# Optimization experiments

Measured on AMD Instinct MI355X. Metric: run time of the kernel, lower is better.

## Reference

```python
import jax, jax.numpy as jnp
import numpy as np
import math

D_MODEL = 1024
D_STATE = 128
D_CONV = 4
EXPAND = 2
HEADDIM = 64
NGROUPS = 1
CHUNK = 256
D_INNER = EXPAND * D_MODEL
D_SSM = D_INNER
NHEADS = D_SSM // HEADDIM
CONV_DIM = D_SSM + 2 * NGROUPS * D_STATE
D_IN_PROJ = 2 * D_INNER + 2 * NGROUPS * D_STATE + NHEADS
BATCH = 2
SEQLEN = 4096
EPS = 1e-5


def segsum(x):
    # x: (..., T) -> (..., T, T); segsum[i, j] = sum_{j < k <= i} x[k], -inf above diagonal
    T = x.shape[-1]
    xc = jnp.cumsum(x, axis=-1)
    d = xc[..., :, None] - xc[..., None, :]
    mask = jnp.tril(jnp.ones((T, T), dtype=bool))
    return jnp.where(mask, d, -jnp.inf)


def setup_inputs() -> dict:
    key = jax.random.key(0)
    ks = jax.random.split(key, 8)
    u = jax.random.normal(ks[0], (BATCH, SEQLEN, D_MODEL), jnp.float32)
    W_in = jax.random.normal(ks[1], (D_IN_PROJ, D_MODEL), jnp.float32) / np.sqrt(D_MODEL)
    conv_w = jax.random.uniform(ks[2], (CONV_DIM, D_CONV), jnp.float32, -1.0, 1.0) / np.sqrt(D_CONV)
    conv_b = jnp.zeros((CONV_DIM,), jnp.float32)
    # dt_bias init as in the torch module: inverse-softplus of dt ~ LogUniform(1e-3, 1e-1)
    dt = jnp.exp(jax.random.uniform(ks[3], (NHEADS,), jnp.float32) * (math.log(0.1) - math.log(0.001)) + math.log(0.001))
    dt = jnp.maximum(dt, 1e-4)
    dt_bias = dt + jnp.log(-jnp.expm1(-dt))
    A_log = jnp.log(jax.random.uniform(ks[4], (NHEADS,), jnp.float32, 1.0, 16.0))
    D = jnp.ones((NHEADS,), jnp.float32)
    norm_w = jnp.ones((D_SSM,), jnp.float32)
    W_out = jax.random.normal(ks[5], (D_MODEL, D_INNER), jnp.float32) / np.sqrt(D_INNER)
    return {"u": u, "W_in": W_in, "conv_w": conv_w, "conv_b": conv_b,
            "dt_bias": dt_bias, "A_log": A_log, "D": D, "norm_w": norm_w, "W_out": W_out}


def reference(u, W_in, conv_w, conv_b, dt_bias, A_log, D, norm_w, W_out):
    b, L, _ = u.shape
    zxbcdt = u @ W_in.T  # (b, L, d_in_proj); d_mlp == 0 for this config
    z, xBC, dt = jnp.split(zxbcdt, [D_SSM, D_SSM + CONV_DIM], axis=-1)

    # depthwise causal conv1d + SiLU (kernel width D_CONV, left padding)
    xpad = jnp.pad(xBC, ((0, 0), (D_CONV - 1, 0), (0, 0)))
    acc = conv_b
    for k in range(D_CONV):
        acc = acc + xpad[:, k:k + L, :] * conv_w[:, k]
    xBC = jax.nn.silu(acc)

    x, Bm, Cm = jnp.split(xBC, [D_SSM, D_SSM + NGROUPS * D_STATE], axis=-1)
    hpg = NHEADS // NGROUPS  # heads per B/C group
    Bh = jnp.repeat(Bm.reshape(b, L, NGROUPS, D_STATE), hpg, axis=2)  # (b, L, h, n)
    Ch = jnp.repeat(Cm.reshape(b, L, NGROUPS, D_STATE), hpg, axis=2)
    x = x.reshape(b, L, NHEADS, HEADDIM)

    dt = jax.nn.softplus(dt + dt_bias)  # (b, L, h)
    A = -jnp.exp(A_log)  # (h,)

    # ---- SSD chunked selective scan ----
    nc = L // CHUNK
    xc = x.reshape(b, nc, CHUNK, NHEADS, HEADDIM)
    Bc = Bh.reshape(b, nc, CHUNK, NHEADS, D_STATE)
    Cc = Ch.reshape(b, nc, CHUNK, NHEADS, D_STATE)
    dt_bclh = dt.reshape(b, nc, CHUNK, NHEADS)
    dA = jnp.transpose(dt_bclh, (0, 3, 1, 2)) * A[None, :, None, None]  # (b, h, c, l)
    A_cs = jnp.cumsum(dA, axis=-1)  # (b, h, c, l)

    # intra-chunk (diagonal block) outputs
    Ldiag = jnp.exp(segsum(dA))  # (b, h, c, l, s)
    x_dt = xc * dt_bclh[..., None]  # fold dt into x
    Y_diag = jnp.einsum('bclhn,bcshn,bhcls,bcshp->bclhp', Cc, Bc, Ldiag, x_dt)

    # per-chunk final states
    decay_states = jnp.exp(A_cs[..., -1:] - A_cs)  # (b, h, c, l)
    states = jnp.einsum('bclhn,bhcl,bclhp->bchpn', Bc, decay_states, x_dt)

    # inter-chunk recurrence via segsum over chunk-level decays
    chunk_sum = jnp.pad(A_cs[..., -1], ((0, 0), (0, 0), (1, 0)))  # (b, h, c+1)
    decay_chunk = jnp.exp(segsum(chunk_sum))  # (b, h, c+1, c+1)
    states = jnp.concatenate([jnp.zeros_like(states[:, :1]), states], axis=1)
    new_states = jnp.einsum('bhzc,bchpn->bzhpn', decay_chunk, states)
    prev_states = new_states[:, :-1]  # state entering each chunk

    # state -> output contribution
    Y_off = jnp.einsum('bclhn,bchpn,bhcl->bclhp', Cc, prev_states, jnp.exp(A_cs))

    y = (Y_diag + Y_off).reshape(b, L, NHEADS, HEADDIM) + x * D[None, None, :, None]
    y = y.reshape(b, L, D_SSM)

    # gated RMSNorm (norm_before_gate=False, ngroups=1 -> full-dim norm)
    y = y * jax.nn.silu(z)
    y = y * jax.lax.rsqrt(jnp.mean(jnp.square(y), axis=-1, keepdims=True) + EPS) * norm_w
    return y @ W_out.T
```

## Files before the change

### kernel.cpp

```cpp
#include <hip/hip_runtime.h>
#include <hip/hip_bf16.h>

#define ZX_LD   4384
#define XC_LD   2304
#define NH      32
#define HD      64
#define DS      128
#define CHK     256
#define NC      16
#define LTOT    4096
#define ROWS    8192
#define DSSM    2048
#define YPAD    80

typedef __bf16 bf16_t;
typedef bf16_t bf16x8 __attribute__((ext_vector_type(8)));
typedef float  f32x4  __attribute__((ext_vector_type(4)));
typedef unsigned short u16x8 __attribute__((ext_vector_type(8)));
typedef unsigned short u16x4 __attribute__((ext_vector_type(4)));

__device__ inline float bf2f(unsigned short u) {
  unsigned int x = ((unsigned int)u) << 16;
  float f; __builtin_memcpy(&f, &x, 4); return f;
}

#define GLOAD_LDS16(gp, lp) \
  __builtin_amdgcn_global_load_lds((const __attribute__((address_space(1))) void*)(gp), \
                                   (__attribute__((address_space(3))) void*)(lp), 16, 0, 0)

__global__ __launch_bounds__(256) void cast_f32_bf16(
    const float* __restrict__ in, bf16_t* __restrict__ out,
    long nvalid, long total)
{
  const long e0 = ((long)blockIdx.x * 256 + threadIdx.x) * 8;
  if (e0 >= total) return;
  bf16x8 o;
  if (e0 + 8 <= nvalid) {
    const float4 a = *(const float4*)(in + e0);
    const float4 b = *(const float4*)(in + e0 + 4);
    o[0]=(bf16_t)a.x; o[1]=(bf16_t)a.y; o[2]=(bf16_t)a.z; o[3]=(bf16_t)a.w;
    o[4]=(bf16_t)b.x; o[5]=(bf16_t)b.y; o[6]=(bf16_t)b.z; o[7]=(bf16_t)b.w;
  } else {
#pragma unroll
    for (int j = 0; j < 8; ++j) o[j] = (bf16_t)0.f;
  }
  *(bf16x8*)(out + e0) = o;
}

__global__ __launch_bounds__(256) void gemm_bt_mfma(
    const bf16_t* __restrict__ A, const bf16_t* __restrict__ B,
    float* __restrict__ C, int M, int N, int K,
    int lda, int ldb, int ldc)
{
  __shared__ __align__(16) bf16_t As[128 * 32];
  __shared__ __align__(16) bf16_t Bs[128 * 32];
  const int tid  = threadIdx.x;
  const int lane = tid & 63;
  const int wave = tid >> 6;

  const int nwg  = gridDim.x * gridDim.y;
  int wgid = blockIdx.y * gridDim.x + blockIdx.x;
  {
    const int xcd = wgid & 7, local = wgid >> 3;
    const int q = nwg >> 3, r = nwg & 7;
    wgid = (xcd < r ? xcd * (q + 1) : r * (q + 1) + (xcd - r) * q) + local;
  }
  const int bm = (wgid / gridDim.x) * 128;
  const int bn = (wgid % gridDim.x) * 128;

  const int wr = (wave >> 1) * 64;
  const int wc = (wave & 1) * 64;

  const int c0   = wave * 2;
  const int lrow = lane >> 2;
  const int lcol = (lane & 3) * 8;
  const bf16_t* Ag0 = A + (size_t)(bm + c0 * 16 + lrow) * lda + lcol;
  const bf16_t* Ag1 = A + (size_t)(bm + c0 * 16 + 16 + lrow) * lda + lcol;
  const bf16_t* Bg0 = B + (size_t)(bn + c0 * 16 + lrow) * ldb + lcol;
  const bf16_t* Bg1 = B + (size_t)(bn + c0 * 16 + 16 + lrow) * ldb + lcol;
  bf16_t* Al0 = As + c0 * 512;
  bf16_t* Al1 = As + c0 * 512 + 512;
  bf16_t* Bl0 = Bs + c0 * 512;
  bf16_t* Bl1 = Bs + c0 * 512 + 512;

  f32x4 acc[4][4];
#pragma unroll
  for (int i = 0; i < 4; ++i)
#pragma unroll
    for (int j = 0; j < 4; ++j) acc[i][j] = (f32x4){0.f, 0.f, 0.f, 0.f};

  const int nk = K >> 5;
  for (int kt = 0; kt < nk; ++kt) {
    const int k0 = kt * 32;
    __syncthreads();
    GLOAD_LDS16(Ag0 + k0, Al0);
    GLOAD_LDS16(Ag1 + k0, Al1);
    GLOAD_LDS16(Bg0 + k0, Bl0);
    GLOAD_LDS16(Bg1 + k0, Bl1);
    __syncthreads();

    const bf16_t* Ab = As + (wr + (lane & 15)) * 32 + (lane >> 4) * 8;
    const bf16_t* Bb = Bs + (wc + (lane & 15)) * 32 + (lane >> 4) * 8;
    bf16x8 af[4], bfv[4];
#pragma unroll
    for (int mi = 0; mi < 4; ++mi) af[mi]  = *(const bf16x8*)(Ab + mi * 512);
#pragma unroll
    for (int ni = 0; ni < 4; ++ni) bfv[ni] = *(const bf16x8*)(Bb + ni * 512);
#pragma unroll
    for (int mi = 0; mi < 4; ++mi)
#pragma unroll
      for (int ni = 0; ni < 4; ++ni)
        acc[mi][ni] = __builtin_amdgcn_mfma_f32_16x16x32_bf16(af[mi], bfv[ni], acc[mi][ni], 0, 0, 0);
  }

  const int crow0 = bm + wr + (lane >> 4) * 4;
  const int ccol0 = bn + wc + (lane & 15);
#pragma unroll
  for (int ni = 0; ni < 4; ++ni) {
    const int ccol = ccol0 + ni * 16;
    if (ccol < N) {
#pragma unroll
      for (int mi = 0; mi < 4; ++mi) {
#pragma unroll
        for (int j = 0; j < 4; ++j) {
          C[(size_t)(crow0 + mi * 16 + j) * ldc + ccol] = acc[mi][ni][j];
        }
      }
    }
  }
}

__global__ __launch_bounds__(256) void conv_silu_kernel(
    const float* __restrict__ zx, const float* __restrict__ cw,
    const float* __restrict__ cb, bf16_t* __restrict__ xconv)
{
  const int ch  = blockIdx.x * 256 + threadIdx.x;
  const int row = blockIdx.y;
  const int l   = row & (LTOT - 1);
  float acc = cb[ch];
#pragma unroll
  for (int k = 0; k < 4; ++k) {
    const int ls = l - 3 + k;
    if (ls >= 0) acc = fmaf(zx[(size_t)(row - 3 + k) * ZX_LD + 2048 + ch], cw[ch*4 + k], acc);
  }
  const float r = acc / (1.f + __expf(-acc));
  xconv[(size_t)row * XC_LD + ch] = (bf16_t)r;
}

__global__ __launch_bounds__(256) void dt_kernel(
    const float* __restrict__ zx, const float* __restrict__ dtb,
    float* __restrict__ dtv)
{
  const int idx = blockIdx.x * 256 + threadIdx.x;
  const int row = idx >> 5;
  const int hh  = idx & 31;
  const float x = zx[(size_t)row * ZX_LD + 4352 + hh] + dtb[hh];
  dtv[idx] = (x > 20.f) ? x : log1pf(__expf(x));
}

__global__ __launch_bounds__(256) void chunk_states_kernel(
    const float* __restrict__ dtv, const float* __restrict__ A_log,
    const bf16_t* __restrict__ xconv,
    float* __restrict__ acs, float* __restrict__ totals,
    float* __restrict__ states)
{
  const int bid = blockIdx.x;
  const int h = bid & 31;
  const int c = (bid >> 5) & 15;
  const int b = bid >> 9;
  const int rowbase = b * LTOT + c * CHK;
  const int tid = threadIdx.x;
  const int lane = tid & 63;
  const int wv   = tid >> 6;
  const int ln15 = lane & 15;
  const int lg   = lane >> 4;

  __shared__ float sWdt[256];
  __shared__ float wsum[4];
  __shared__ __align__(16) bf16_t xT[64 * 64];
  __shared__ __align__(16) bf16_t Bt[128 * 64];
  unsigned short* Btu = (unsigned short*)Bt;

  const float dt = dtv[(size_t)(rowbase + tid) * NH + h];
  const float Ah = -__expf(A_log[h]);
  float v = dt * Ah;
#pragma unroll
  for (int off = 1; off < 64; off <<= 1) {
    float up = __shfl_up(v, off, 64);
    if ((tid & 63) >= off) v += up;
  }
  if ((tid & 63) == 63) wsum[tid >> 6] = v;
  __syncthreads();
  const float w0 = wsum[0], w1 = wsum[1], w2 = wsum[2], w3 = wsum[3];
  float base = 0.f;
  if (wv > 0) base += w0;
  if (wv > 1) base += w1;
  if (wv > 2) base += w2;
  const float acsl  = v + base;
  const float total = w0 + w1 + w2 + w3;
  acs[bid * 256 + tid] = acsl;
  if (tid == 0) totals[(b * 32 + h) * 16 + c] = total;
  sWdt[tid] = __expf(total - acsl) * dt;

  f32x4 acc[4][2];
#pragma unroll
  for (int i = 0; i < 4; ++i)
#pragma unroll
    for (int j = 0; j < 2; ++j) acc[i][j] = (f32x4){0.f, 0.f, 0.f, 0.f};

  const int s  = tid >> 2;
  const int p0 = (tid & 3) * 16;
  const int n0 = (tid & 3) * 32;

  for (int ls = 0; ls < 4; ++ls) {
    const int l0 = ls * 64;
    __syncthreads();
    {
      const float wgt = sWdt[l0 + s];
      const bf16_t* xr = xconv + (size_t)(rowbase + l0 + s) * XC_LD + h * HD + p0;
      u16x8 v0 = *(const u16x8*)xr;
      u16x8 v1 = *(const u16x8*)(xr + 8);
#pragma unroll
      for (int j = 0; j < 8; ++j) {
        const int p = p0 + j;
        xT[p * 64 + ((((s >> 3) ^ (p & 7)) << 3) | (s & 7))] = (bf16_t)(bf2f(v0[j]) * wgt);
      }
#pragma unroll
      for (int j = 0; j < 8; ++j) {
        const int p = p0 + 8 + j;
        xT[p * 64 + ((((s >> 3) ^ (p & 7)) << 3) | (s & 7))] = (bf16_t)(bf2f(v1[j]) * wgt);
      }
      const bf16_t* br = xconv + (size_t)(rowbase + l0 + s) * XC_LD + 2048 + n0;
#pragma unroll
      for (int q = 0; q < 4; ++q) {
        u16x8 t = *(const u16x8*)(br + q * 8);
#pragma unroll
        for (int j = 0; j < 8; ++j) {
          const int n = n0 + q * 8 + j;
          Btu[n * 64 + ((((s >> 3) ^ (n & 7)) << 3) | (s & 7))] = t[j];
        }
      }
    }
    __syncthreads();
#pragma unroll
    for (int ks = 0; ks < 2; ++ks) {
      bf16x8 af[4];
#pragma unroll
      for (int mi = 0; mi < 4; ++mi) {
        const int row = mi * 16 + ln15;
        const int chunk = (ks * 4 + lg) ^ (row & 7);
        af[mi] = *(const bf16x8*)(xT + row * 64 + chunk * 8);
      }
#pragma unroll
      for (int ni = 0; ni < 2; ++ni) {
        const int nrow = wv * 32 + ni * 16 + ln15;
        const int chunk = (ks * 4 + lg) ^ (nrow & 7);
        bf16x8 bfr = *(const bf16x8*)(Bt + nrow * 64 + chunk * 8);
#pragma unroll
        for (int mi = 0; mi < 4; ++mi)
          acc[mi][ni] = __builtin_amdgcn_mfma_f32_16x16x32_bf16(af[mi], bfr, acc[mi][ni], 0, 0, 0);
      }
    }
  }

  const size_t sbase = (size_t)bid * (HD * DS);
#pragma unroll
  for (int mi = 0; mi < 4; ++mi) {
#pragma unroll
    for (int ni = 0; ni < 2; ++ni) {
      const int n = wv * 32 + ni * 16 + ln15;
#pragma unroll
      for (int j = 0; j < 4; ++j) {
        const int p = mi * 16 + lg * 4 + j;
        states[sbase + p * DS + n] = acc[mi][ni][j];
      }
    }
  }
}

__global__ __launch_bounds__(256) void chunk_prefix_kernel(
    const float* __restrict__ st, const float* __restrict__ totals,
    bf16_t* __restrict__ prevbf)
{
  const int bh = blockIdx.x;
  const int b = bh >> 5;
  const int h = bh & 31;
  const int e = blockIdx.y;
  const int tid = threadIdx.x;
  float P = 0.f;
  for (int c = 0; c < NC; ++c) {
    const size_t idx = (size_t)((b * 16 + c) * 32 + h) * (HD * DS) + e * 256 + tid;
    const float g = __expf(totals[bh * 16 + c]);
    prevbf[idx] = (bf16_t)P;
    P = fmaf(P, g, st[idx]);
  }
}

__global__ __launch_bounds__(256) void y_kernel_mfma(
    const bf16_t* __restrict__ xconv, const float* __restrict__ dtv,
    const float* __restrict__ acs,   const bf16_t* __restrict__ prevbf,
    const float* __restrict__ Dv,    float* __restrict__ ypre, int ypld)
{
  const int bid = blockIdx.x;
  const int lt = bid & 3;
  const int h  = (bid >> 2) & 31;
  const int c  = (bid >> 7) & 15;
  const int b  = bid >> 11;
  const int bch = (b * 16 + c) * 32 + h;
  const int rowbase = b * LTOT + c * CHK;
  const int tid  = threadIdx.x;
  const int lane = tid & 63;
  const int wv   = tid >> 6;
  const int ln15 = lane & 15;
  const int lg   = lane >> 4;

  __shared__ float sAcs[256];
  __shared__ float sDt[256];
  __shared__ __align__(16) bf16_t Cl[64 * 128];
  __shared__ __align__(16) bf16_t Bl[64 * 128];
  __shared__ __align__(16) bf16_t Sl[64 * YPAD];
  __shared__ __align__(16) bf16_t xT[64 * YPAD];
  unsigned short* xTu = (unsigned short*)xT;

  sAcs[tid] = acs[bch * 256 + tid];
  sDt[tid]  = dtv[(size_t)(rowbase + tid) * NH + h];

#pragma unroll
  for (int i = 0; i < 4; ++i) {
    const int chunk = wv * 4 + i;
    const int r  = chunk * 4 + lg;
    const int cs = ln15 ^ (r & 7);
    const bf16_t* src = xconv + (size_t)(rowbase + lt*64 + r) * XC_LD + 2176 + cs * 8;
    GLOAD_LDS16(src, Cl + chunk * 512);
  }
  __syncthreads();

  bf16x8 cf[4][4];
#pragma unroll
  for (int mi = 0; mi < 4; ++mi) {
    const int row = mi * 16 + ln15;
#pragma unroll
    for (int ks = 0; ks < 4; ++ks) {
      const int chunk = (ks * 4 + lg) ^ (row & 7);
      cf[mi][ks] = *(const bf16x8*)(Cl + row * 128 + chunk * 8);
    }
  }

  f32x4 acc[4];
#pragma unroll
  for (int mi = 0; mi < 4; ++mi) acc[mi] = (f32x4){0.f, 0.f, 0.f, 0.f};
  {
    const bf16_t* pb = prevbf + ((size_t)bch * 64 + 16 * wv + ln15) * 128 + lg * 8;
#pragma unroll
    for (int ks = 0; ks < 4; ++ks) {
      bf16x8 pf = *(const bf16x8*)(pb + ks * 32);
#pragma unroll
      for (int mi = 0; mi < 4; ++mi)
        acc[mi] = __builtin_amdgcn_mfma_f32_16x16x32_bf16(cf[mi][ks], pf, acc[mi], 0, 0, 0);
    }
  }
#pragma unroll
  for (int mi = 0; mi < 4; ++mi) {
#pragma unroll
    for (int j = 0; j < 4; ++j)
      acc[mi][j] *= __expf(sAcs[lt*64 + mi*16 + lg*4 + j]);
  }

  for (int st = 0; st <= lt; ++st) {
    __syncthreads();
#pragma unroll
    for (int i = 0; i < 4; ++i) {
      const int chunk = wv * 4 + i;
      const int r  = chunk * 4 + lg;
      const int cs = ln15 ^ (r & 7);
      const bf16_t* src = xconv + (size_t)(rowbase + st*64 + r) * XC_LD + 2048 + cs * 8;
      GLOAD_LDS16(src, Bl + chunk * 512);
    }
    {
      const int s  = tid >> 2;
      const int p0 = (tid & 3) * 16;
      const bf16_t* xr = xconv + (size_t)(rowbase + st*64 + s) * XC_LD + h * HD + p0;
      u16x8 v0 = *(const u16x8*)xr;
      u16x8 v1 = *(const u16x8*)(xr + 8);
#pragma unroll
      for (int j = 0; j < 8; ++j) xTu[(p0 + j) * YPAD + s] = v0[j];
#pragma unroll
      for (int j = 0; j < 8; ++j) xTu[(p0 + 8 + j) * YPAD + s] = v1[j];
    }
    __syncthreads();

    f32x4 sa[4];
#pragma unroll
    for (int mi = 0; mi < 4; ++mi) sa[mi] = (f32x4){0.f, 0.f, 0.f, 0.f};
    {
      const int row = 16 * wv + ln15;
#pragma unroll
      for (int ks = 0; ks < 4; ++ks) {
        const int chunk = (ks * 4 + lg) ^ (row & 7);
        bf16x8 bfr = *(const bf16x8*)(Bl + row * 128 + chunk * 8);
#pragma unroll
        for (int mi = 0; mi < 4; ++mi)
          sa[mi] = __builtin_amdgcn_mfma_f32_16x16x32_bf16(cf[mi][ks], bfr, sa[mi], 0, 0, 0);
      }
    }
    {
      const int sg = st * 64 + 16 * wv + ln15;
      const float as  = sAcs[sg];
      const float dts = sDt[sg];
#pragma unroll
      for (int mi = 0; mi < 4; ++mi) {
#pragma unroll
        for (int j = 0; j < 4; ++j) {
          const int lloc = mi * 16 + lg * 4 + j;
          const int ll = lt * 64 + lloc;
          float wvv = 0.f;
          if (ll >= sg) wvv = sa[mi][j] * __expf(sAcs[ll] - as) * dts;
          Sl[lloc * YPAD + 16 * wv + ln15] = (bf16_t)wvv;
        }
      }
    }
    __syncthreads();

#pragma unroll
    for (int ks2 = 0; ks2 < 2; ++ks2) {
      bf16x8 xf = *(const bf16x8*)(xT + (16 * wv + ln15) * YPAD + ks2 * 32 + lg * 8);
#pragma unroll
      for (int mi = 0; mi < 4; ++mi) {
        bf16x8 sf = *(const bf16x8*)(Sl + (mi * 16 + ln15) * YPAD + ks2 * 32 + lg * 8);
        acc[mi] = __builtin_amdgcn_mfma_f32_16x16x32_bf16(sf, xf, acc[mi], 0, 0, 0);
      }
    }
  }

  const float Dh = Dv[h];
  const int p = 16 * wv + ln15;
#pragma unroll
  for (int mi = 0; mi < 4; ++mi) {
#pragma unroll
    for (int j = 0; j < 4; ++j) {
      const int lloc = mi * 16 + lg * 4 + j;
      const int row  = rowbase + lt * 64 + lloc;
      const float xv = (float)xT[p * YPAD + lloc];
      ypre[(size_t)row * ypld + h * HD + p] = acc[mi][j] + xv * Dh;
    }
  }
}

__global__ __launch_bounds__(256) void rmsnorm_gate_kernel(
    const float* __restrict__ zx, const float* __restrict__ normw,
    bf16_t* __restrict__ ypre_bf)
{
  const int row = blockIdx.x;
  const int tid = threadIdx.x;
  float vals[8];
  float ss = 0.f;
#pragma unroll
  for (int e = 0; e < 8; ++e) {
    const int col = e * 256 + tid;
    const float y = zx[(size_t)row * ZX_LD + 2048 + col];
    const float z = zx[(size_t)row * ZX_LD + col];
    const float sz = z / (1.f + __expf(-z));
    const float v = y * sz;
    vals[e] = v;
    ss += v * v;
  }
#pragma unroll
  for (int off = 32; off >= 1; off >>= 1) ss += __shfl_xor(ss, off, 64);
  __shared__ float red[4];
  if ((tid & 63) == 0) red[tid >> 6] = ss;
  __syncthreads();
  const float tot = red[0] + red[1] + red[2] + red[3];
  const float scale = rsqrtf(tot / (float)DSSM + 1e-5f);
#pragma unroll
  for (int e = 0; e < 8; ++e) {
    const int col = e * 256 + tid;
    ypre_bf[(size_t)row * DSSM + col] = (bf16_t)(vals[e] * scale * normw[col]);
  }
}

extern "C" void kernel_launch(void* const* d_in, const int* in_sizes, int n_in,
                              void* d_out, int out_size, void* d_ws, size_t ws_size,
                              hipStream_t stream)
{
  const float* u       = (const float*)d_in[0];
  const float* W_in    = (const float*)d_in[1];
  const float* conv_w  = (const float*)d_in[2];
  const float* conv_b  = (const float*)d_in[3];
  const float* dt_bias = (const float*)d_in[4];
  const float* A_log   = (const float*)d_in[5];
  const float* Dv      = (const float*)d_in[6];
  const float* norm_w  = (const float*)d_in[7];
  const float* W_out   = (const float*)d_in[8];
  float* out = (float*)d_out;

  const size_t OFF_XC  = (size_t)ROWS * ZX_LD * 4;
  const size_t OFF_DT  = OFF_XC  + (size_t)ROWS * XC_LD * 2;
  const size_t OFF_ACS = OFF_DT  + (size_t)ROWS * NH * 4;
  const size_t OFF_TOT = OFF_ACS + (size_t)1024 * 256 * 4;
  const size_t OFF_ST  = OFF_TOT + 4096;
  const size_t OFF_AR  = OFF_ST  + (size_t)1024 * HD * DS * 4;
  const size_t need    = OFF_AR  + (size_t)ROWS * XC_LD * 2;
  if (ws_size < need) return;

  char* w = (char*)d_ws;
  float*  zx      = (float*)w;
  bf16_t* xconv   = (bf16_t*)(w + OFF_XC);
  float*  dtv     = (float*)(w + OFF_DT);
  float*  acsb    = (float*)(w + OFF_ACS);
  float*  totals  = (float*)(w + OFF_TOT);
  float*  states  = (float*)(w + OFF_ST);
  bf16_t* arena   = (bf16_t*)(w + OFF_AR);
  bf16_t* u_bf    = arena;
  bf16_t* Wpad    = arena + (size_t)ROWS * 1024;
  bf16_t* prevbf  = arena;
  bf16_t* ypre_bf = arena;
  bf16_t* Wout_bf = arena + (size_t)ROWS * DSSM;
  float*  ypre    = zx + 2048;

  {
    const long n_u = (long)ROWS * 1024;
    cast_f32_bf16<<<dim3((n_u/8 + 255)/256), 256, 0, stream>>>(u, u_bf, n_u, n_u);
    const long n_wv = (long)4384 * 1024, n_wt = (long)4480 * 1024;
    cast_f32_bf16<<<dim3((n_wt/8 + 255)/256), 256, 0, stream>>>(W_in, Wpad, n_wv, n_wt);
    const long n_wo = (long)1024 * DSSM;
    cast_f32_bf16<<<dim3((n_wo/8 + 255)/256), 256, 0, stream>>>(W_out, Wout_bf, n_wo, n_wo);
  }
  gemm_bt_mfma<<<dim3(35, 64), 256, 0, stream>>>(u_bf, Wpad, zx, ROWS, 4384, 1024,
                                                 1024, 1024, ZX_LD);
  conv_silu_kernel<<<dim3(9, ROWS), 256, 0, stream>>>(zx, conv_w, conv_b, xconv);
  dt_kernel<<<dim3((ROWS * NH) / 256), 256, 0, stream>>>(zx, dt_bias, dtv);
  chunk_states_kernel<<<dim3(1024), 256, 0, stream>>>(dtv, A_log, xconv, acsb, totals, states);
  chunk_prefix_kernel<<<dim3(64, 32), 256, 0, stream>>>(states, totals, prevbf);
  y_kernel_mfma<<<dim3(4096), 256, 0, stream>>>(xconv, dtv, acsb, prevbf, Dv, ypre, ZX_LD);
  rmsnorm_gate_kernel<<<dim3(ROWS), 256, 0, stream>>>(zx, norm_w, ypre_bf);
  gemm_bt_mfma<<<dim3(8, 64), 256, 0, stream>>>(ypre_bf, Wout_bf, out, ROWS, 1024, 2048,
                                                2048, 2048, 1024);
}
```

Baseline: 525.2 us.

## Store in_proj output and y intermediate in bf16, drop LDS staging in y kernel

The in_proj GEMM now writes its zxbcdt result as bf16 instead of fp32, halving the intermediate buffer. The conv, dt, y and rmsnorm kernels read and write bf16 versions of it. The rmsnorm kernel switches to vectorised 8-wide loads and stores. The y kernel drops its LDS staging for C and B and loads MFMA operands straight from global memory, removing one barrier per step. This cuts memory traffic but loses precision in z, dt and the y intermediate, and direct global fragment loads may be less coalesced than the previous staged path.

```diff
diff --git a/kernel.cpp b/kernel.cpp
--- a/kernel.cpp
+++ b/kernel.cpp
@@ -17,7 +17,6 @@
 typedef bf16_t bf16x8 __attribute__((ext_vector_type(8)));
 typedef float  f32x4  __attribute__((ext_vector_type(4)));
 typedef unsigned short u16x8 __attribute__((ext_vector_type(8)));
-typedef unsigned short u16x4 __attribute__((ext_vector_type(4)));
 
 __device__ inline float bf2f(unsigned short u) {
   unsigned int x = ((unsigned int)u) << 16;
@@ -47,9 +46,10 @@
   *(bf16x8*)(out + e0) = o;
 }
 
+template<bool BF16OUT>
 __global__ __launch_bounds__(256) void gemm_bt_mfma(
     const bf16_t* __restrict__ A, const bf16_t* __restrict__ B,
-    float* __restrict__ C, int M, int N, int K,
+    void* __restrict__ Cv, int M, int N, int K,
     int lda, int ldb, int ldc)
 {
   __shared__ __align__(16) bf16_t As[128 * 32];
@@ -123,7 +123,11 @@
       for (int mi = 0; mi < 4; ++mi) {
 #pragma unroll
         for (int j = 0; j < 4; ++j) {
-          C[(size_t)(crow0 + mi * 16 + j) * ldc + ccol] = acc[mi][ni][j];
+          if constexpr (BF16OUT) {
+            ((bf16_t*)Cv)[(size_t)(crow0 + mi * 16 + j) * ldc + ccol] = (bf16_t)acc[mi][ni][j];
+          } else {
+            ((float*)Cv)[(size_t)(crow0 + mi * 16 + j) * ldc + ccol] = acc[mi][ni][j];
+          }
         }
       }
     }
@@ -131,7 +135,7 @@
 }
 
 __global__ __launch_bounds__(256) void conv_silu_kernel(
-    const float* __restrict__ zx, const float* __restrict__ cw,
+    const bf16_t* __restrict__ zx, const float* __restrict__ cw,
     const float* __restrict__ cb, bf16_t* __restrict__ xconv)
 {
   const int ch  = blockIdx.x * 256 + threadIdx.x;
@@ -141,20 +145,21 @@
 #pragma unroll
   for (int k = 0; k < 4; ++k) {
     const int ls = l - 3 + k;
-    if (ls >= 0) acc = fmaf(zx[(size_t)(row - 3 + k) * ZX_LD + 2048 + ch], cw[ch*4 + k], acc);
+    if (ls >= 0)
+      acc = fmaf((float)zx[(size_t)(row - 3 + k) * ZX_LD + 2048 + ch], cw[ch*4 + k], acc);
   }
   const float r = acc / (1.f + __expf(-acc));
   xconv[(size_t)row * XC_LD + ch] = (bf16_t)r;
 }
 
 __global__ __launch_bounds__(256) void dt_kernel(
-    const float* __restrict__ zx, const float* __restrict__ dtb,
+    const bf16_t* __restrict__ zx, const float* __restrict__ dtb,
     float* __restrict__ dtv)
 {
   const int idx = blockIdx.x * 256 + threadIdx.x;
   const int row = idx >> 5;
   const int hh  = idx & 31;
-  const float x = zx[(size_t)row * ZX_LD + 4352 + hh] + dtb[hh];
+  const float x = (float)zx[(size_t)row * ZX_LD + 4352 + hh] + dtb[hh];
   dtv[idx] = (x > 20.f) ? x : log1pf(__expf(x));
 }
 
@@ -299,7 +304,7 @@
 __global__ __launch_bounds__(256) void y_kernel_mfma(
     const bf16_t* __restrict__ xconv, const float* __restrict__ dtv,
     const float* __restrict__ acs,   const bf16_t* __restrict__ prevbf,
-    const float* __restrict__ Dv,    float* __restrict__ ypre, int ypld)
+    const float* __restrict__ Dv,    bf16_t* __restrict__ ypre, int ypld)
 {
   const int bid = blockIdx.x;
   const int lt = bid & 3;
@@ -316,34 +321,20 @@
 
   __shared__ float sAcs[256];
   __shared__ float sDt[256];
-  __shared__ __align__(16) bf16_t Cl[64 * 128];
-  __shared__ __align__(16) bf16_t Bl[64 * 128];
   __shared__ __align__(16) bf16_t Sl[64 * YPAD];
   __shared__ __align__(16) bf16_t xT[64 * YPAD];
   unsigned short* xTu = (unsigned short*)xT;
 
   sAcs[tid] = acs[bch * 256 + tid];
   sDt[tid]  = dtv[(size_t)(rowbase + tid) * NH + h];
-
-#pragma unroll
-  for (int i = 0; i < 4; ++i) {
-    const int chunk = wv * 4 + i;
-    const int r  = chunk * 4 + lg;
-    const int cs = ln15 ^ (r & 7);
-    const bf16_t* src = xconv + (size_t)(rowbase + lt*64 + r) * XC_LD + 2176 + cs * 8;
-    GLOAD_LDS16(src, Cl + chunk * 512);
-  }
   __syncthreads();
 
   bf16x8 cf[4][4];
 #pragma unroll
   for (int mi = 0; mi < 4; ++mi) {
-    const int row = mi * 16 + ln15;
-#pragma unroll
-    for (int ks = 0; ks < 4; ++ks) {
-      const int chunk = (ks * 4 + lg) ^ (row & 7);
-      cf[mi][ks] = *(const bf16x8*)(Cl + row * 128 + chunk * 8);
-    }
+    const bf16_t* crow = xconv + (size_t)(rowbase + lt*64 + mi*16 + ln15) * XC_LD + 2176 + lg * 8;
+#pragma unroll
+    for (int ks = 0; ks < 4; ++ks) cf[mi][ks] = *(const bf16x8*)(crow + ks * 32);
   }
 
   f32x4 acc[4];
@@ -368,14 +359,6 @@
 
   for (int st = 0; st <= lt; ++st) {
     __syncthreads();
-#pragma unroll
-    for (int i = 0; i < 4; ++i) {
-      const int chunk = wv * 4 + i;
-      const int r  = chunk * 4 + lg;
-      const int cs = ln15 ^ (r & 7);
-      const bf16_t* src = xconv + (size_t)(rowbase + st*64 + r) * XC_LD + 2048 + cs * 8;
-      GLOAD_LDS16(src, Bl + chunk * 512);
-    }
     {
       const int s  = tid >> 2;
       const int p0 = (tid & 3) * 16;
@@ -387,17 +370,15 @@
 #pragma unroll
       for (int j = 0; j < 8; ++j) xTu[(p0 + 8 + j) * YPAD + s] = v1[j];
     }
-    __syncthreads();
 
     f32x4 sa[4];
 #pragma unroll
     for (int mi = 0; mi < 4; ++mi) sa[mi] = (f32x4){0.f, 0.f, 0.f, 0.f};
     {
-      const int row = 16 * wv + ln15;
+      const bf16_t* brow = xconv + (size_t)(rowbase + st*64 + 16*wv + ln15) * XC_LD + 2048 + lg * 8;
 #pragma unroll
       for (int ks = 0; ks < 4; ++ks) {
-        const int chunk = (ks * 4 + lg) ^ (row & 7);
-        bf16x8 bfr = *(const bf16x8*)(Bl + row * 128 + chunk * 8);
+        bf16x8 bfr = *(const bf16x8*)(brow + ks * 32);
 #pragma unroll
         for (int mi = 0; mi < 4; ++mi)
           sa[mi] = __builtin_amdgcn_mfma_f32_16x16x32_bf16(cf[mi][ks], bfr, sa[mi], 0, 0, 0);
@@ -441,27 +422,29 @@
       const int lloc = mi * 16 + lg * 4 + j;
       const int row  = rowbase + lt * 64 + lloc;
       const float xv = (float)xT[p * YPAD + lloc];
-      ypre[(size_t)row * ypld + h * HD + p] = acc[mi][j] + xv * Dh;
+      ypre[(size_t)row * ypld + h * HD + p] = (bf16_t)(acc[mi][j] + xv * Dh);
     }
   }
 }
 
 __global__ __launch_bounds__(256) void rmsnorm_gate_kernel(
-    const float* __restrict__ zx, const float* __restrict__ normw,
+    const bf16_t* __restrict__ zx, const float* __restrict__ normw,
     bf16_t* __restrict__ ypre_bf)
 {
   const int row = blockIdx.x;
   const int tid = threadIdx.x;
+  const unsigned short* zr = (const unsigned short*)(zx + (size_t)row * ZX_LD);
+  u16x8 yv = *(const u16x8*)(zr + 2048 + tid * 8);
+  u16x8 zv = *(const u16x8*)(zr + tid * 8);
   float vals[8];
   float ss = 0.f;
 #pragma unroll
-  for (int e = 0; e < 8; ++e) {
-    const int col = e * 256 + tid;
-    const float y = zx[(size_t)row * ZX_LD + 2048 + col];
-    const float z = zx[(size_t)row * ZX_LD + col];
+  for (int j = 0; j < 8; ++j) {
+    const float y = bf2f(yv[j]);
+    const float z = bf2f(zv[j]);
     const float sz = z / (1.f + __expf(-z));
     const float v = y * sz;
-    vals[e] = v;
+    vals[j] = v;
     ss += v * v;
   }
 #pragma unroll
@@ -471,11 +454,18 @@
   __syncthreads();
   const float tot = red[0] + red[1] + red[2] + red[3];
   const float scale = rsqrtf(tot / (float)DSSM + 1e-5f);
-#pragma unroll
-  for (int e = 0; e < 8; ++e) {
-    const int col = e * 256 + tid;
-    ypre_bf[(size_t)row * DSSM + col] = (bf16_t)(vals[e] * scale * normw[col]);
-  }
+  const float4 w0 = *(const float4*)(normw + tid * 8);
+  const float4 w1 = *(const float4*)(normw + tid * 8 + 4);
+  bf16x8 o;
+  o[0] = (bf16_t)(vals[0] * scale * w0.x);
+  o[1] = (bf16_t)(vals[1] * scale * w0.y);
+  o[2] = (bf16_t)(vals[2] * scale * w0.z);
+  o[3] = (bf16_t)(vals[3] * scale * w0.w);
+  o[4] = (bf16_t)(vals[4] * scale * w1.x);
+  o[5] = (bf16_t)(vals[5] * scale * w1.y);
+  o[6] = (bf16_t)(vals[6] * scale * w1.z);
+  o[7] = (bf16_t)(vals[7] * scale * w1.w);
+  *(bf16x8*)(ypre_bf + (size_t)row * DSSM + tid * 8) = o;
 }
 
 extern "C" void kernel_launch(void* const* d_in, const int* in_sizes, int n_in,
@@ -493,7 +483,7 @@
   const float* W_out   = (const float*)d_in[8];
   float* out = (float*)d_out;
 
-  const size_t OFF_XC  = (size_t)ROWS * ZX_LD * 4;
+  const size_t OFF_XC  = (size_t)ROWS * ZX_LD * 2;
   const size_t OFF_DT  = OFF_XC  + (size_t)ROWS * XC_LD * 2;
   const size_t OFF_ACS = OFF_DT  + (size_t)ROWS * NH * 4;
   const size_t OFF_TOT = OFF_ACS + (size_t)1024 * 256 * 4;
@@ -503,7 +493,7 @@
   if (ws_size < need) return;
 
   char* w = (char*)d_ws;
-  float*  zx      = (float*)w;
+  bf16_t* zxb     = (bf16_t*)w;
   bf16_t* xconv   = (bf16_t*)(w + OFF_XC);
   float*  dtv     = (float*)(w + OFF_DT);
   float*  acsb    = (float*)(w + OFF_ACS);
@@ -515,7 +505,7 @@
   bf16_t* prevbf  = arena;
   bf16_t* ypre_bf = arena;
   bf16_t* Wout_bf = arena + (size_t)ROWS * DSSM;
-  float*  ypre    = zx + 2048;
+  bf16_t* ypre_ov = zxb + 2048;
 
   {
     const long n_u = (long)ROWS * 1024;
@@ -525,14 +515,14 @@
     const long n_wo = (long)1024 * DSSM;
     cast_f32_bf16<<<dim3((n_wo/8 + 255)/256), 256, 0, stream>>>(W_out, Wout_bf, n_wo, n_wo);
   }
-  gemm_bt_mfma<<<dim3(35, 64), 256, 0, stream>>>(u_bf, Wpad, zx, ROWS, 4384, 1024,
-                                                 1024, 1024, ZX_LD);
-  conv_silu_kernel<<<dim3(9, ROWS), 256, 0, stream>>>(zx, conv_w, conv_b, xconv);
-  dt_kernel<<<dim3((ROWS * NH) / 256), 256, 0, stream>>>(zx, dt_bias, dtv);
+  gemm_bt_mfma<true><<<dim3(35, 64), 256, 0, stream>>>(u_bf, Wpad, zxb, ROWS, 4384, 1024,
+                                                       1024, 1024, ZX_LD);
+  conv_silu_kernel<<<dim3(9, ROWS), 256, 0, stream>>>(zxb, conv_w, conv_b, xconv);
+  dt_kernel<<<dim3((ROWS * NH) / 256), 256, 0, stream>>>(zxb, dt_bias, dtv);
   chunk_states_kernel<<<dim3(1024), 256, 0, stream>>>(dtv, A_log, xconv, acsb, totals, states);
   chunk_prefix_kernel<<<dim3(64, 32), 256, 0, stream>>>(states, totals, prevbf);
-  y_kernel_mfma<<<dim3(4096), 256, 0, stream>>>(xconv, dtv, acsb, prevbf, Dv, ypre, ZX_LD);
-  rmsnorm_gate_kernel<<<dim3(ROWS), 256, 0, stream>>>(zx, norm_w, ypre_bf);
-  gemm_bt_mfma<<<dim3(8, 64), 256, 0, stream>>>(ypre_bf, Wout_bf, out, ROWS, 1024, 2048,
-                                                2048, 2048, 1024);
-}
+  y_kernel_mfma<<<dim3(4096), 256, 0, stream>>>(xconv, dtv, acsb, prevbf, Dv, ypre_ov, ZX_LD);
+  rmsnorm_gate_kernel<<<dim3(ROWS), 256, 0, stream>>>(zxb, norm_w, ypre_bf);
+  gemm_bt_mfma<false><<<dim3(8, 64), 256, 0, stream>>>(ypre_bf, Wout_bf, out, ROWS, 1024, 2048,
+                                                       2048, 2048, 1024);
+}
```

New measurement: 508.3 us. 3.2% less time.
